# Kernel optimization log

Measured on AMD Instinct MI355X. Metric: run time of the kernel, lower is better.

## Reference

```python
import jax, jax.numpy as jnp
import numpy as np

N_NODES = 100_000
N_HYPEREDGES = 200_000
NNZ = 2_000_000
D = 64
H = 32
KEEP_RATIO = 0.5


def setup_inputs() -> dict:
    key = jax.random.key(0)
    ks = jax.random.split(key, 5)
    x = jax.random.normal(ks[0], (N_NODES, D), jnp.float32)
    V_idx = jax.random.randint(ks[1], (NNZ,), 0, N_NODES)
    E_idx = jax.random.randint(ks[2], (NNZ,), 0, N_HYPEREDGES)
    W1 = jax.random.normal(ks[3], (2 * D, H), jnp.float32) * (1.0 / np.sqrt(2 * D))
    b1 = jnp.zeros((H,), jnp.float32)
    W2 = jax.random.normal(ks[4], (H, 1), jnp.float32) * (1.0 / np.sqrt(H))
    b2 = jnp.zeros((1,), jnp.float32)
    return dict(x=x, V_idx=V_idx, E_idx=E_idx, W1=W1, b1=b1, W2=W2, b2=b2)


def _segment_mean(vals, idx, num_segments):
    # index_add sum / clamped count, matching reduce_incidence_to_edge / index_mean
    s = jax.ops.segment_sum(vals, idx, num_segments=num_segments)
    c = jax.ops.segment_sum(jnp.ones((vals.shape[0],), vals.dtype), idx,
                            num_segments=num_segments)
    c = jnp.clip(c, 1.0, None)
    if vals.ndim == 2:
        c = c[:, None]
    return s / c


def reference(x, V_idx, E_idx, W1, b1, W2, b2):
    xv = x[V_idx]                                   # [nnz, D] gather
    edge_feats = _segment_mean(xv, E_idx, N_HYPEREDGES)  # [E, D]
    pair = jnp.concatenate([xv, edge_feats[E_idx]], axis=-1)  # [nnz, 2D]
    h = jax.nn.relu(pair @ W1 + b1)                 # [nnz, H]
    probs = jax.nn.sigmoid((h @ W2 + b2)[:, 0])     # [nnz]

    k = max(1, int(KEEP_RATIO * NNZ))
    keep_ids = jax.lax.top_k(probs, k)[1]           # is_test=True path (deterministic)
    hard = jnp.zeros_like(probs).at[keep_ids].set(1.0)
    soft = jax.lax.stop_gradient(hard - probs) + probs  # straight-through

    edge_probs = _segment_mean(jax.lax.stop_gradient(probs), E_idx, N_HYPEREDGES)
    edge_soft = _segment_mean(soft, E_idx, N_HYPEREDGES)
    edge_hard = (_segment_mean(hard, E_idx, N_HYPEREDGES) > 0).astype(jnp.float32)
    return (probs, soft, hard, edge_probs, edge_soft, edge_hard)
```

## Files before the change

### kernel.cpp

```cpp
#include <hip/hip_runtime.h>
#include <math.h>

#define N_NODES   100000
#define N_EDGES   200000
#define NNZ       2000000
#define K_KEEP    1000000
#define BANDCAP   131072
#define TIECAP    4096
#define DELTA     1.0e-3f
#define SCAN_BLOCKS 196
#define USCALE (4294967296.0 / 4.0e-3)

#define OFF_PAB   ((size_t)0)
#define OFF_PB32  ((size_t)25600000)
#define OFF_VJ    ((size_t)33600000)
#define OFF_POS   ((size_t)49600000)
#define OFF_EOFF  ((size_t)57600000)
#define OFF_CUR   ((size_t)58400000)
#define OFF_BS    ((size_t)59200000)
#define OFF_BANDP ((size_t)59201024)
#define OFF_BANDJ ((size_t)59725312)
#define OFF_BANDE ((size_t)60249600)
#define OFF_BANDV ((size_t)60773888)
#define OFF_BANDK ((size_t)61298176)
#define OFF_TIEK  ((size_t)62346752)
#define OFF_TIEJ  ((size_t)62379520)
#define OFF_TIEP  ((size_t)62395904)
#define OFF_FLAG  ((size_t)62412288)
#define OFF_ECNT  ((size_t)64412288)
#define OFF_HIST  ((size_t)65212288)
#define OFF_ST    ((size_t)65245056)
#define ZERO_OFF  OFF_FLAG
#define ZERO_LEN  ((size_t)(65245312 - 62412288))

struct SelState {
    unsigned int B1;
    unsigned int rem1;
    float lo_edge, hi_edge;
    unsigned int bB1;
    unsigned int brem1;
    unsigned int bU0;
    unsigned int brem2;
    unsigned int _pad0[8];
    unsigned int n_hi;      unsigned int _pad1[15];
    unsigned int band_n;    unsigned int _pad2[15];
    unsigned int tie_n;     unsigned int _pad3[15];
};

__device__ __forceinline__ unsigned int band_u32(double key, float lo) {
    double t = (key - (double)lo) * USCALE;
    t = t < 0.0 ? 0.0 : (t > 4294967295.0 ? 4294967295.0 : t);
    return (unsigned int)t;
}

__global__ void proj_kernel(const float* __restrict__ x, const float* __restrict__ W1,
                            float2* __restrict__ p_ab2) {
    __shared__ float sW[128 * 32];
    __shared__ float sx[8][64];
    for (int t = threadIdx.x; t < 128 * 32; t += 256) sW[t] = W1[t];
    int base = blockIdx.x * 8;
    for (int t = threadIdx.x; t < 512; t += 256) {
        int n = t >> 6, d = t & 63;
        int g = base + n;
        sx[n][d] = (g < N_NODES) ? x[(size_t)g * 64 + d] : 0.f;
    }
    __syncthreads();
    int ln = threadIdx.x >> 5;
    int k  = threadIdx.x & 31;
    int node = base + ln;
    if (node >= N_NODES) return;
    float sa = 0.f, sb = 0.f;
    for (int d = 0; d < 64; ++d) {
        float xv = sx[ln][d];
        sa += xv * sW[d * 32 + k];
        sb += xv * sW[(64 + d) * 32 + k];
    }
    p_ab2[(size_t)node * 32 + k] = make_float2(sa, sb);
}

__global__ void count_kernel(const int* __restrict__ E, unsigned int* __restrict__ edge_cnt) {
    int j = blockIdx.x * 256 + threadIdx.x;
    if (j >= NNZ) return;
    atomicAdd(&edge_cnt[E[j]], 1u);
}

__global__ void scanA_kernel(const unsigned int* __restrict__ edge_cnt,
                             unsigned int* __restrict__ edge_off, unsigned int* __restrict__ bsums) {
    __shared__ unsigned int s[256];
    int tid = threadIdx.x;
    int base = blockIdx.x * 1024 + tid * 4;
    unsigned int v0 = (base + 0 < N_EDGES) ? edge_cnt[base + 0] : 0u;
    unsigned int v1 = (base + 1 < N_EDGES) ? edge_cnt[base + 1] : 0u;
    unsigned int v2 = (base + 2 < N_EDGES) ? edge_cnt[base + 2] : 0u;
    unsigned int v3 = (base + 3 < N_EDGES) ? edge_cnt[base + 3] : 0u;
    unsigned int tsum = v0 + v1 + v2 + v3;
    s[tid] = tsum;
    __syncthreads();
    for (int off = 1; off < 256; off <<= 1) {
        unsigned int t = (tid >= off) ? s[tid - off] : 0u;
        __syncthreads();
        s[tid] += t;
        __syncthreads();
    }
    unsigned int excl = s[tid] - tsum;
    if (base + 0 < N_EDGES) edge_off[base + 0] = excl;
    if (base + 1 < N_EDGES) edge_off[base + 1] = excl + v0;
    if (base + 2 < N_EDGES) edge_off[base + 2] = excl + v0 + v1;
    if (base + 3 < N_EDGES) edge_off[base + 3] = excl + v0 + v1 + v2;
    if (tid == 255) bsums[blockIdx.x] = s[255];
}

__global__ void scanB_kernel(unsigned int* __restrict__ bsums) {
    __shared__ unsigned int s[256];
    int tid = threadIdx.x;
    unsigned int v = (tid < SCAN_BLOCKS) ? bsums[tid] : 0u;
    s[tid] = v;
    __syncthreads();
    for (int off = 1; off < 256; off <<= 1) {
        unsigned int t = (tid >= off) ? s[tid - off] : 0u;
        __syncthreads();
        s[tid] += t;
        __syncthreads();
    }
    if (tid < SCAN_BLOCKS) bsums[tid] = s[tid] - v;
}

__global__ void scanC_kernel(unsigned int* __restrict__ edge_off, const unsigned int* __restrict__ bsums,
                             unsigned int* __restrict__ cursor) {
    int i = blockIdx.x * 256 + threadIdx.x;
    if (i >= N_EDGES) return;
    unsigned int o = edge_off[i] + bsums[i >> 10];
    edge_off[i] = o;
    cursor[i] = o;
}

__global__ void bucket_kernel(const int* __restrict__ V, const int* __restrict__ E,
                              unsigned int* __restrict__ cursor,
                              uint2* __restrict__ vj, unsigned int* __restrict__ pos) {
    unsigned int base = blockIdx.x * 2048 + threadIdx.x;
    int ev[8], vv[8];
    unsigned int pp[8];
    #pragma unroll
    for (int c = 0; c < 8; ++c) {
        unsigned int j = base + 256u * c;
        if (j < NNZ) { ev[c] = E[j]; vv[c] = V[j]; }
    }
    #pragma unroll
    for (int c = 0; c < 8; ++c) {
        unsigned int j = base + 256u * c;
        if (j < NNZ) pp[c] = atomicAdd(&cursor[ev[c]], 1u);
    }
    #pragma unroll
    for (int c = 0; c < 8; ++c) {
        unsigned int j = base + 256u * c;
        if (j < NNZ) {
            vj[pp[c]] = make_uint2((unsigned int)vv[c], j);
            pos[j] = pp[c];
        }
    }
}

__global__ void edge_logit_kernel(const uint2* __restrict__ vj,
                                  const unsigned int* __restrict__ edge_off,
                                  const unsigned int* __restrict__ edge_cnt,
                                  const float2* __restrict__ p_ab2,
                                  const float* __restrict__ b1, const float* __restrict__ W2,
                                  const float* __restrict__ b2,
                                  float* __restrict__ probs_b, float* __restrict__ o_ep) {
    __shared__ float sa[4][32 * 32];
    __shared__ float slog[4][32];
    __shared__ unsigned int sv[4][32];
    int e = blockIdx.x * 4 + (threadIdx.x >> 6);
    if (e >= N_EDGES) return;
    int w    = threadIdx.x >> 6;
    int lane = threadIdx.x & 63;
    int k    = lane & 31;
    unsigned int half = (unsigned int)(lane >> 5);

    unsigned int off = edge_off[e];
    unsigned int deg = edge_cnt[e];
    unsigned int mind = deg < 32u ? deg : 32u;

    if ((unsigned int)lane < mind) sv[w][lane] = vj[off + lane].x;

    float bacc = 0.f;
    unsigned int i = half;
    for (; i + 6u < mind; i += 8u) {
        unsigned int v0 = sv[w][i];
        unsigned int v1 = sv[w][i + 2u];
        unsigned int v2 = sv[w][i + 4u];
        unsigned int v3 = sv[w][i + 6u];
        float2 r0 = p_ab2[(size_t)v0 * 32u + k];
        float2 r1 = p_ab2[(size_t)v1 * 32u + k];
        float2 r2 = p_ab2[(size_t)v2 * 32u + k];
        float2 r3 = p_ab2[(size_t)v3 * 32u + k];
        sa[w][(i)      * 32 + k] = r0.x;
        sa[w][(i + 2u) * 32 + k] = r1.x;
        sa[w][(i + 4u) * 32 + k] = r2.x;
        sa[w][(i + 6u) * 32 + k] = r3.x;
        bacc += (r0.y + r1.y) + (r2.y + r3.y);
    }
    for (; i + 2u < mind; i += 4u) {
        unsigned int v0 = sv[w][i];
        unsigned int v1 = sv[w][i + 2u];
        float2 r0 = p_ab2[(size_t)v0 * 32u + k];
        float2 r1 = p_ab2[(size_t)v1 * 32u + k];
        sa[w][(i)      * 32 + k] = r0.x;
        sa[w][(i + 2u) * 32 + k] = r1.x;
        bacc += r0.y + r1.y;
    }
    for (; i < mind; i += 2u) {
        unsigned int v = sv[w][i];
        float2 r = p_ab2[(size_t)v * 32u + k];
        sa[w][i * 32 + k] = r.x;
        bacc += r.y;
    }
    for (i = 32u + half; i < deg; i += 2u) {
        unsigned int v = vj[off + i].x;
        bacc += p_ab2[(size_t)v * 32u + k].y;
    }

    float cc  = (float)(deg > 1u ? deg : 1u);
    float emk = (bacc + __shfl_xor(bacc, 32)) / cc + b1[k];
    float w2k = W2[k];
    float b2v = b2[0];
    float prsum = 0.f;

    i = half;
    for (; i + 2u < mind; i += 4u) {
        float h0 = sa[w][(i)      * 32 + k] + emk;
        float h1 = sa[w][(i + 2u) * 32 + k] + emk;
        h0 = h0 > 0.f ? h0 : 0.f;
        h1 = h1 > 0.f ? h1 : 0.f;
        float t0 = h0 * w2k;
        float t1 = h1 * w2k;
        #pragma unroll
        for (int o = 16; o > 0; o >>= 1) {
            t0 += __shfl_down(t0, o, 32);
            t1 += __shfl_down(t1, o, 32);
        }
        if (k == 0) { slog[w][i] = t0; slog[w][i + 2u] = t1; }
    }
    for (; i < mind; i += 2u) {
        float hk = sa[w][i * 32 + k] + emk;
        hk = hk > 0.f ? hk : 0.f;
        float t = hk * w2k;
        #pragma unroll
        for (int o = 16; o > 0; o >>= 1) t += __shfl_down(t, o, 32);
        if (k == 0) slog[w][i] = t;
    }
    if ((unsigned int)lane < mind) {
        float pr = 1.f / (1.f + __expf(-(slog[w][lane] + b2v)));
        probs_b[off + lane] = pr;
        prsum = pr;
    }
    for (i = 32u + half; i < deg; i += 2u) {
        unsigned int v = vj[off + i].x;
        float hk = p_ab2[(size_t)v * 32u + k].x + emk;
        hk = hk > 0.f ? hk : 0.f;
        float t = hk * w2k;
        #pragma unroll
        for (int o = 16; o > 0; o >>= 1) t += __shfl_down(t, o, 32);
        if (k == 0) {
            float pr = 1.f / (1.f + __expf(-(t + b2v)));
            probs_b[off + i] = pr;
            prsum += pr;
        }
    }
    #pragma unroll
    for (int o = 32; o > 0; o >>= 1) prsum += __shfl_down(prsum, o, 64);
    if (lane == 0) o_ep[e] = prsum / cc;
}

__global__ void hist1_kernel(const float* __restrict__ probs_b, unsigned int* __restrict__ hist) {
    __shared__ unsigned int lh[2048];
    for (int t = threadIdx.x; t < 2048; t += 256) lh[t] = 0;
    __syncthreads();
    for (unsigned int i = blockIdx.x * 256 + threadIdx.x; i < NNZ; i += gridDim.x * 256) {
        unsigned int key = __float_as_uint(probs_b[i]);
        atomicAdd(&lh[key >> 21], 1u);
    }
    __syncthreads();
    for (int t = threadIdx.x; t < 2048; t += 256)
        if (lh[t]) atomicAdd(&hist[t], lh[t]);
}

__global__ void hist2_kernel(const float* __restrict__ probs_b, const SelState* __restrict__ st,
                             unsigned int* __restrict__ hist) {
    __shared__ unsigned int lh[2048];
    for (int t = threadIdx.x; t < 2048; t += 256) lh[t] = 0;
    __syncthreads();
    unsigned int B1 = st->B1;
    for (unsigned int i = blockIdx.x * 256 + threadIdx.x; i < NNZ; i += gridDim.x * 256) {
        unsigned int key = __float_as_uint(probs_b[i]);
        if ((key >> 21) == B1) atomicAdd(&lh[(key >> 10) & 2047u], 1u);
    }
    __syncthreads();
    for (int t = threadIdx.x; t < 2048; t += 256)
        if (lh[t]) atomicAdd(&hist[2048 + t], lh[t]);
}

__global__ void scan_sel_kernel(const unsigned int* __restrict__ hist, SelState* __restrict__ st, int which) {
    __shared__ unsigned int csum[256];
    int t = threadIdx.x;
    unsigned int target = (which == 0) ? (unsigned int)K_KEEP : st->rem1;
    const unsigned int* h = hist + (which ? 2048 : 0);
    unsigned int b[8];
    unsigned int s = 0;
    #pragma unroll
    for (int i = 0; i < 8; ++i) { b[i] = h[t * 8 + i]; s += b[i]; }
    csum[t] = s;
    __syncthreads();
    for (int off = 1; off < 256; off <<= 1) {
        unsigned int v = (t + off < 256) ? csum[t + off] : 0u;
        __syncthreads();
        csum[t] += v;
        __syncthreads();
    }
    unsigned int above = csum[t] - s;
    if (above < target && target <= above + s) {
        unsigned int rem = target - above;
        unsigned int cum = 0;
        #pragma unroll
        for (int i = 7; i >= 0; --i) {
            if (rem <= cum + b[i]) {
                unsigned int bin = (unsigned int)(t * 8 + i);
                if (which == 0) { st->B1 = bin; st->rem1 = rem - cum; }
                else {
                    unsigned int P = (st->B1 << 21) | (bin << 10);
                    st->lo_edge = __uint_as_float(P) - DELTA;
                    st->hi_edge = __uint_as_float(P + 1024u) + DELTA;
                }
                break;
            }
            cum += b[i];
        }
    }
}

__global__ void bandsel_kernel(const float* __restrict__ probs_b, const int* __restrict__ E,
                               const uint2* __restrict__ vj,
                               SelState* __restrict__ st,
                               unsigned int* __restrict__ band_p, unsigned int* __restrict__ band_j,
                               unsigned int* __restrict__ band_e, unsigned int* __restrict__ band_v) {
    __shared__ unsigned int whi[4], wband[4];
    __shared__ unsigned int sbase, scur;
    float hi = st->hi_edge, lo = st->lo_edge;
    unsigned int nhi = 0, nband = 0;
    for (unsigned int p = blockIdx.x * 256 + threadIdx.x; p < NNZ; p += gridDim.x * 256) {
        float pk = probs_b[p];
        if (pk > hi) nhi++;
        else if (pk >= lo) nband++;
    }
    #pragma unroll
    for (int o = 32; o > 0; o >>= 1) {
        nhi   += __shfl_down(nhi, o);
        nband += __shfl_down(nband, o);
    }
    if ((threadIdx.x & 63) == 0) { whi[threadIdx.x >> 6] = nhi; wband[threadIdx.x >> 6] = nband; }
    __syncthreads();
    if (threadIdx.x == 0) {
        unsigned int th = whi[0] + whi[1] + whi[2] + whi[3];
        unsigned int tb = wband[0] + wband[1] + wband[2] + wband[3];
        if (th) atomicAdd(&st->n_hi, th);
        sbase = tb ? atomicAdd(&st->band_n, tb) : 0u;
        scur = 0;
    }
    __syncthreads();
    for (unsigned int p = blockIdx.x * 256 + threadIdx.x; p < NNZ; p += gridDim.x * 256) {
        float pk = probs_b[p];
        if (pk <= hi && pk >= lo) {
            unsigned int s = sbase + atomicAdd(&scur, 1u);
            if (s < BANDCAP) {
                uint2 t = vj[p];
                band_p[s] = p;
                band_j[s] = t.y;
                band_e[s] = (unsigned int)E[t.y];
                band_v[s] = t.x;
            }
        }
    }
}

__global__ void rescue_kernel(const uint2* __restrict__ vj,
                              const unsigned int* __restrict__ edge_off,
                              const unsigned int* __restrict__ edge_cnt,
                              const float* __restrict__ x, const float* __restrict__ W1,
                              const float* __restrict__ b1, const float* __restrict__ W2,
                              const float* __restrict__ b2,
                              const unsigned int* __restrict__ band_e,
                              const unsigned int* __restrict__ band_v,
                              const SelState* __restrict__ st,
                              unsigned long long* __restrict__ band_key) {
    unsigned int n = st->band_n; if (n > BANDCAP) n = BANDCAP;
    if (blockIdx.x * 8 >= n) return;
    __shared__ float sW[128 * 32];
    for (int t = threadIdx.x; t < 128 * 32; t += 256) sW[t] = W1[t];
    __syncthreads();
    unsigned int g = blockIdx.x * 8 + (threadIdx.x >> 5);
    if (g >= n) return;
    int k = threadIdx.x & 31;
    unsigned int v = band_v[g];
    unsigned int e = band_e[g];
    unsigned int off = edge_off[e];
    unsigned int deg = edge_cnt[e];

    const float* xv = x + (size_t)v * 64u;
    double a = 0.0;
    #pragma unroll 8
    for (int d = 0; d < 64; ++d) a += (double)xv[d] * (double)sW[d * 32 + k];
    double bsum = 0.0;
    for (unsigned int m = off; m < off + deg; ++m) {
        const float* xm = x + (size_t)vj[m].x * 64u;
        double acc = 0.0;
        #pragma unroll 8
        for (int d = 0; d < 64; ++d) acc += (double)xm[d] * (double)sW[(64 + d) * 32 + k];
        bsum += acc;
    }
    double cc = (double)(deg > 1u ? deg : 1u);
    double h = a + bsum / cc + (double)b1[k];
    h = h > 0.0 ? h : 0.0;
    double t = h * (double)W2[k];
    #pragma unroll
    for (int o = 16; o > 0; o >>= 1) t += __shfl_down(t, o, 32);
    if (k == 0) {
        double pr = 1.0 / (1.0 + exp(-(t + (double)b2[0])));
        band_key[g] = (unsigned long long)__double_as_longlong(pr);
    }
}

__global__ void bhist1_kernel(const unsigned long long* __restrict__ band_key,
                              const SelState* __restrict__ st, unsigned int* __restrict__ hist) {
    __shared__ unsigned int lh[2048];
    for (int t = threadIdx.x; t < 2048; t += 256) lh[t] = 0;
    __syncthreads();
    unsigned int n = st->band_n; if (n > BANDCAP) n = BANDCAP;
    float lo = st->lo_edge;
    for (unsigned int i = blockIdx.x * 256 + threadIdx.x; i < n; i += gridDim.x * 256) {
        unsigned int u = band_u32(__longlong_as_double((long long)band_key[i]), lo);
        atomicAdd(&lh[u >> 21], 1u);
    }
    __syncthreads();
    for (int t = threadIdx.x; t < 2048; t += 256)
        if (lh[t]) atomicAdd(&hist[4096 + t], lh[t]);
}

__global__ void bhist2_kernel(const unsigned long long* __restrict__ band_key,
                              const SelState* __restrict__ st, unsigned int* __restrict__ hist) {
    __shared__ unsigned int lh[2048];
    for (int t = threadIdx.x; t < 2048; t += 256) lh[t] = 0;
    __syncthreads();
    unsigned int n = st->band_n; if (n > BANDCAP) n = BANDCAP;
    float lo = st->lo_edge;
    unsigned int bB1 = st->bB1;
    for (unsigned int i = blockIdx.x * 256 + threadIdx.x; i < n; i += gridDim.x * 256) {
        unsigned int u = band_u32(__longlong_as_double((long long)band_key[i]), lo);
        if ((u >> 21) == bB1) atomicAdd(&lh[(u >> 10) & 2047u], 1u);
    }
    __syncthreads();
    for (int t = threadIdx.x; t < 2048; t += 256)
        if (lh[t]) atomicAdd(&hist[6144 + t], lh[t]);
}

__global__ void bscan_kernel(const unsigned int* __restrict__ hist, SelState* __restrict__ st, int which) {
    __shared__ unsigned int csum[256];
    int t = threadIdx.x;
    unsigned int target = (which == 0) ? ((unsigned int)K_KEEP - st->n_hi) : st->brem1;
    const unsigned int* h = hist + (which ? 6144 : 4096);
    unsigned int b[8];
    unsigned int s = 0;
    #pragma unroll
    for (int i = 0; i < 8; ++i) { b[i] = h[t * 8 + i]; s += b[i]; }
    csum[t] = s;
    __syncthreads();
    for (int off = 1; off < 256; off <<= 1) {
        unsigned int v = (t + off < 256) ? csum[t + off] : 0u;
        __syncthreads();
        csum[t] += v;
        __syncthreads();
    }
    unsigned int above = csum[t] - s;
    if (above < target && target <= above + s) {
        unsigned int rem = target - above;
        unsigned int cum = 0;
        #pragma unroll
        for (int i = 7; i >= 0; --i) {
            if (rem <= cum + b[i]) {
                unsigned int bin = (unsigned int)(t * 8 + i);
                if (which == 0) { st->bB1 = bin; st->brem1 = rem - cum; }
                else            { st->bU0 = (st->bB1 << 21) | (bin << 10); st->brem2 = rem - cum; }
                break;
            }
            cum += b[i];
        }
    }
}

__global__ void btie_kernel(const unsigned long long* __restrict__ band_key,
                            const unsigned int* __restrict__ band_j,
                            const unsigned int* __restrict__ band_p,
                            SelState* __restrict__ st, unsigned char* __restrict__ flag,
                            unsigned long long* __restrict__ tie_k,
                            unsigned int* __restrict__ tie_j, unsigned int* __restrict__ tie_p) {
    unsigned int n = st->band_n; if (n > BANDCAP) n = BANDCAP;
    unsigned int i = blockIdx.x * 256 + threadIdx.x;
    if (i >= n) return;
    float lo = st->lo_edge;
    unsigned int U0 = st->bU0;
    unsigned long long key = band_key[i];
    unsigned int u = band_u32(__longlong_as_double((long long)key), lo);
    if (u >= U0 + 1024u) {
        flag[band_p[i]] = 2u;
    } else if (u >= U0) {
        unsigned int s = atomicAdd(&st->tie_n, 1u);
        if (s < TIECAP) { tie_k[s] = key; tie_j[s] = band_j[i]; tie_p[s] = band_p[i]; }
    }
}

__global__ void btierank_kernel(const unsigned long long* __restrict__ tie_k,
                                const unsigned int* __restrict__ tie_j,
                                const unsigned int* __restrict__ tie_p,
                                const SelState* __restrict__ st, unsigned char* __restrict__ flag) {
    unsigned int n = st->tie_n; if (n > TIECAP) n = TIECAP;
    unsigned int need = st->brem2;
    for (unsigned int i = threadIdx.x; i < n; i += 256) {
        unsigned long long ki = tie_k[i];
        unsigned int ji = tie_j[i];
        unsigned int r = 0;
        for (unsigned int q = 0; q < n; ++q) {
            unsigned long long kq = tie_k[q];
            if (kq > ki || (kq == ki && tie_j[q] < ji)) r++;
        }
        if (r < need) flag[tie_p[i]] = 2u;
    }
}

__global__ void out_kernel(const float* __restrict__ probs_b, const unsigned char* __restrict__ flag,
                           const unsigned int* __restrict__ pos, const SelState* __restrict__ st,
                           float* __restrict__ o_probs, float* __restrict__ o_soft, float* __restrict__ o_hard) {
    unsigned int j = blockIdx.x * 256 + threadIdx.x;
    if (j >= NNZ) return;
    float hi = st->hi_edge;
    unsigned int p = pos[j];
    float pk = probs_b[p];
    float hb = (pk > hi || flag[p] == 2u) ? 1.f : 0.f;
    o_probs[j] = pk;
    o_soft[j]  = hb;
    o_hard[j]  = hb;
}

__global__ void edge_out_kernel(const float* __restrict__ probs_b, const unsigned char* __restrict__ flag,
                                const unsigned int* __restrict__ edge_off,
                                const unsigned int* __restrict__ edge_cnt,
                                const SelState* __restrict__ st,
                                float* __restrict__ o_es, float* __restrict__ o_eh) {
    unsigned int e = blockIdx.x * 256 + threadIdx.x;
    if (e >= N_EDGES) return;
    float hi = st->hi_edge;
    unsigned int off = edge_off[e], deg = edge_cnt[e];
    unsigned int cnt = 0;
    for (unsigned int i = 0; i < deg; ++i)
        cnt += (probs_b[off + i] > hi || flag[off + i] == 2u) ? 1u : 0u;
    float cc = (float)(deg > 1u ? deg : 1u);
    o_es[e] = (float)cnt / cc;
    o_eh[e] = cnt ? 1.f : 0.f;
}

extern "C" void kernel_launch(void* const* d_in, const int* in_sizes, int n_in,
                              void* d_out, int out_size, void* d_ws, size_t ws_size,
                              hipStream_t stream) {
    const float* x  = (const float*)d_in[0];
    const int*   V  = (const int*)d_in[1];
    const int*   E  = (const int*)d_in[2];
    const float* W1 = (const float*)d_in[3];
    const float* b1 = (const float*)d_in[4];
    const float* W2 = (const float*)d_in[5];
    const float* b2 = (const float*)d_in[6];

    float* out     = (float*)d_out;
    float* o_probs = out;
    float* o_soft  = out + NNZ;
    float* o_hard  = out + 2 * (size_t)NNZ;
    float* o_ep    = out + 3 * (size_t)NNZ;
    float* o_es    = out + 3 * (size_t)NNZ + N_EDGES;
    float* o_eh    = out + 3 * (size_t)NNZ + 2 * (size_t)N_EDGES;

    char* w = (char*)d_ws;
    float2*             p_ab2    = (float2*)(w + OFF_PAB);
    float*              probs_b  = (float*)(w + OFF_PB32);
    uint2*              vj       = (uint2*)(w + OFF_VJ);
    unsigned int*       pos      = (unsigned int*)(w + OFF_POS);
    unsigned int*       edge_off = (unsigned int*)(w + OFF_EOFF);
    unsigned int*       cursor   = (unsigned int*)(w + OFF_CUR);
    unsigned int*       bsums    = (unsigned int*)(w + OFF_BS);
    unsigned int*       band_p   = (unsigned int*)(w + OFF_BANDP);
    unsigned int*       band_j   = (unsigned int*)(w + OFF_BANDJ);
    unsigned int*       band_e   = (unsigned int*)(w + OFF_BANDE);
    unsigned int*       band_v   = (unsigned int*)(w + OFF_BANDV);
    unsigned long long* band_key = (unsigned long long*)(w + OFF_BANDK);
    unsigned long long* tie_k    = (unsigned long long*)(w + OFF_TIEK);
    unsigned int*       tie_j    = (unsigned int*)(w + OFF_TIEJ);
    unsigned int*       tie_p    = (unsigned int*)(w + OFF_TIEP);
    unsigned char*      flag     = (unsigned char*)(w + OFF_FLAG);
    unsigned int*       edge_cnt = (unsigned int*)(w + OFF_ECNT);
    unsigned int*       hist     = (unsigned int*)(w + OFF_HIST);
    SelState*           st       = (SelState*)(w + OFF_ST);

    hipMemsetAsync(w + ZERO_OFF, 0, ZERO_LEN, stream);

    proj_kernel<<<(N_NODES + 7) / 8, 256, 0, stream>>>(x, W1, p_ab2);

    count_kernel<<<(NNZ + 255) / 256, 256, 0, stream>>>(E, edge_cnt);
    scanA_kernel<<<SCAN_BLOCKS, 256, 0, stream>>>(edge_cnt, edge_off, bsums);
    scanB_kernel<<<1, 256, 0, stream>>>(bsums);
    scanC_kernel<<<(N_EDGES + 255) / 256, 256, 0, stream>>>(edge_off, bsums, cursor);
    bucket_kernel<<<(NNZ + 2047) / 2048, 256, 0, stream>>>(V, E, cursor, vj, pos);

    edge_logit_kernel<<<(N_EDGES + 3) / 4, 256, 0, stream>>>(vj, edge_off, edge_cnt,
                                                             p_ab2, b1, W2, b2, probs_b, o_ep);

    hist1_kernel<<<1024, 256, 0, stream>>>(probs_b, hist);
    scan_sel_kernel<<<1, 256, 0, stream>>>(hist, st, 0);
    hist2_kernel<<<1024, 256, 0, stream>>>(probs_b, st, hist);
    scan_sel_kernel<<<1, 256, 0, stream>>>(hist, st, 1);

    bandsel_kernel<<<1024, 256, 0, stream>>>(probs_b, E, vj, st,
                                             band_p, band_j, band_e, band_v);
    rescue_kernel<<<BANDCAP / 8, 256, 0, stream>>>(vj, edge_off, edge_cnt, x, W1, b1, W2, b2,
                                                   band_e, band_v, st, band_key);

    bhist1_kernel<<<64, 256, 0, stream>>>(band_key, st, hist);
    bscan_kernel<<<1, 256, 0, stream>>>(hist, st, 0);
    bhist2_kernel<<<64, 256, 0, stream>>>(band_key, st, hist);
    bscan_kernel<<<1, 256, 0, stream>>>(hist, st, 1);
    btie_kernel<<<BANDCAP / 256, 256, 0, stream>>>(band_key, band_j, band_p, st, flag,
                                                   tie_k, tie_j, tie_p);
    btierank_kernel<<<1, 256, 0, stream>>>(tie_k, tie_j, tie_p, st, flag);

    out_kernel<<<(NNZ + 255) / 256, 256, 0, stream>>>(probs_b, flag, pos, st, o_probs, o_soft, o_hard);
    edge_out_kernel<<<(N_EDGES + 255) / 256, 256, 0, stream>>>(probs_b, flag, edge_off, edge_cnt, st,
                                                               o_es, o_eh);
}
```

Baseline: 672.2 us.

## Compute bucket ranks during counting and scatter in edge-range passes

The counting kernel now records each incidence's rank within its edge from the atomicAdd return value, so the separate cursor atomics in the bucket kernel go away. A new scatter kernel writes vj positions as offset plus rank, split into 8 passes by edge range so each pass's scattered writes land in a smaller region for better cache locality. The pos array is dropped and out_kernel recomputes the position from E, rank and edge_off. This adds repeated streaming reads of E (eight passes) and extra gathers in out_kernel in exchange for fewer atomics and more localized writes.

```diff
diff --git a/kernel.cpp b/kernel.cpp
--- a/kernel.cpp
+++ b/kernel.cpp
@@ -11,10 +11,14 @@
 #define SCAN_BLOCKS 196
 #define USCALE (4294967296.0 / 4.0e-3)
 
+#define SC_PASSES 8
+#define SC_EPP    (N_EDGES / SC_PASSES)
+#define SC_BLOCKS 2048
+
 #define OFF_PAB   ((size_t)0)
 #define OFF_PB32  ((size_t)25600000)
 #define OFF_VJ    ((size_t)33600000)
-#define OFF_POS   ((size_t)49600000)
+#define OFF_RANK  ((size_t)49600000)
 #define OFF_EOFF  ((size_t)57600000)
 #define OFF_CUR   ((size_t)58400000)
 #define OFF_BS    ((size_t)59200000)
@@ -78,10 +82,26 @@
     p_ab2[(size_t)node * 32 + k] = make_float2(sa, sb);
 }
 
-__global__ void count_kernel(const int* __restrict__ E, unsigned int* __restrict__ edge_cnt) {
-    int j = blockIdx.x * 256 + threadIdx.x;
-    if (j >= NNZ) return;
-    atomicAdd(&edge_cnt[E[j]], 1u);
+__global__ void count_rank_kernel(const int* __restrict__ E, unsigned int* __restrict__ edge_cnt,
+                                  unsigned int* __restrict__ rank) {
+    unsigned int base = blockIdx.x * 2048 + threadIdx.x;
+    int ev[8];
+    unsigned int rr[8];
+    #pragma unroll
+    for (int c = 0; c < 8; ++c) {
+        unsigned int j = base + 256u * c;
+        if (j < NNZ) ev[c] = E[j];
+    }
+    #pragma unroll
+    for (int c = 0; c < 8; ++c) {
+        unsigned int j = base + 256u * c;
+        if (j < NNZ) rr[c] = atomicAdd(&edge_cnt[ev[c]], 1u);
+    }
+    #pragma unroll
+    for (int c = 0; c < 8; ++c) {
+        unsigned int j = base + 256u * c;
+        if (j < NNZ) rank[j] = rr[c];
+    }
 }
 
 __global__ void scanA_kernel(const unsigned int* __restrict__ edge_cnt,
@@ -125,37 +145,26 @@
     if (tid < SCAN_BLOCKS) bsums[tid] = s[tid] - v;
 }
 
-__global__ void scanC_kernel(unsigned int* __restrict__ edge_off, const unsigned int* __restrict__ bsums,
-                             unsigned int* __restrict__ cursor) {
+__global__ void scanC_kernel(unsigned int* __restrict__ edge_off, const unsigned int* __restrict__ bsums) {
     int i = blockIdx.x * 256 + threadIdx.x;
     if (i >= N_EDGES) return;
-    unsigned int o = edge_off[i] + bsums[i >> 10];
-    edge_off[i] = o;
-    cursor[i] = o;
-}
-
-__global__ void bucket_kernel(const int* __restrict__ V, const int* __restrict__ E,
-                              unsigned int* __restrict__ cursor,
-                              uint2* __restrict__ vj, unsigned int* __restrict__ pos) {
-    unsigned int base = blockIdx.x * 2048 + threadIdx.x;
-    int ev[8], vv[8];
-    unsigned int pp[8];
-    #pragma unroll
-    for (int c = 0; c < 8; ++c) {
-        unsigned int j = base + 256u * c;
-        if (j < NNZ) { ev[c] = E[j]; vv[c] = V[j]; }
-    }
-    #pragma unroll
-    for (int c = 0; c < 8; ++c) {
-        unsigned int j = base + 256u * c;
-        if (j < NNZ) pp[c] = atomicAdd(&cursor[ev[c]], 1u);
-    }
-    #pragma unroll
-    for (int c = 0; c < 8; ++c) {
-        unsigned int j = base + 256u * c;
-        if (j < NNZ) {
-            vj[pp[c]] = make_uint2((unsigned int)vv[c], j);
-            pos[j] = pp[c];
+    edge_off[i] = edge_off[i] + bsums[i >> 10];
+}
+
+__global__ void scatter_kernel(const int* __restrict__ V, const int* __restrict__ E,
+                               const unsigned int* __restrict__ edge_off,
+                               const unsigned int* __restrict__ rank,
+                               uint2* __restrict__ vj) {
+    unsigned int pass = blockIdx.x & 7u;
+    unsigned int q    = blockIdx.x >> 3;
+    unsigned int elo  = pass * SC_EPP;
+    const unsigned int stride = (SC_BLOCKS / 8) * 256;
+    for (unsigned int j = q * 256u + threadIdx.x; j < NNZ; j += stride) {
+        unsigned int e = (unsigned int)__builtin_nontemporal_load(E + j);
+        if (e - elo < (unsigned int)SC_EPP) {
+            unsigned int pp = edge_off[e] + __builtin_nontemporal_load(rank + j);
+            unsigned int v  = (unsigned int)__builtin_nontemporal_load(V + j);
+            vj[pp] = make_uint2(v, j);
         }
     }
 }
@@ -536,12 +545,13 @@
 }
 
 __global__ void out_kernel(const float* __restrict__ probs_b, const unsigned char* __restrict__ flag,
-                           const unsigned int* __restrict__ pos, const SelState* __restrict__ st,
+                           const int* __restrict__ E, const unsigned int* __restrict__ rank,
+                           const unsigned int* __restrict__ edge_off, const SelState* __restrict__ st,
                            float* __restrict__ o_probs, float* __restrict__ o_soft, float* __restrict__ o_hard) {
     unsigned int j = blockIdx.x * 256 + threadIdx.x;
     if (j >= NNZ) return;
     float hi = st->hi_edge;
-    unsigned int p = pos[j];
+    unsigned int p = edge_off[E[j]] + rank[j];
     float pk = probs_b[p];
     float hb = (pk > hi || flag[p] == 2u) ? 1.f : 0.f;
     o_probs[j] = pk;
@@ -589,9 +599,8 @@
     float2*             p_ab2    = (float2*)(w + OFF_PAB);
     float*              probs_b  = (float*)(w + OFF_PB32);
     uint2*              vj       = (uint2*)(w + OFF_VJ);
-    unsigned int*       pos      = (unsigned int*)(w + OFF_POS);
+    unsigned int*       rank     = (unsigned int*)(w + OFF_RANK);
     unsigned int*       edge_off = (unsigned int*)(w + OFF_EOFF);
-    unsigned int*       cursor   = (unsigned int*)(w + OFF_CUR);
     unsigned int*       bsums    = (unsigned int*)(w + OFF_BS);
     unsigned int*       band_p   = (unsigned int*)(w + OFF_BANDP);
     unsigned int*       band_j   = (unsigned int*)(w + OFF_BANDJ);
@@ -610,11 +619,11 @@
 
     proj_kernel<<<(N_NODES + 7) / 8, 256, 0, stream>>>(x, W1, p_ab2);
 
-    count_kernel<<<(NNZ + 255) / 256, 256, 0, stream>>>(E, edge_cnt);
+    count_rank_kernel<<<(NNZ + 2047) / 2048, 256, 0, stream>>>(E, edge_cnt, rank);
     scanA_kernel<<<SCAN_BLOCKS, 256, 0, stream>>>(edge_cnt, edge_off, bsums);
     scanB_kernel<<<1, 256, 0, stream>>>(bsums);
-    scanC_kernel<<<(N_EDGES + 255) / 256, 256, 0, stream>>>(edge_off, bsums, cursor);
-    bucket_kernel<<<(NNZ + 2047) / 2048, 256, 0, stream>>>(V, E, cursor, vj, pos);
+    scanC_kernel<<<(N_EDGES + 255) / 256, 256, 0, stream>>>(edge_off, bsums);
+    scatter_kernel<<<SC_BLOCKS, 256, 0, stream>>>(V, E, edge_off, rank, vj);
 
     edge_logit_kernel<<<(N_EDGES + 3) / 4, 256, 0, stream>>>(vj, edge_off, edge_cnt,
                                                              p_ab2, b1, W2, b2, probs_b, o_ep);
@@ -637,7 +646,8 @@
                                                    tie_k, tie_j, tie_p);
     btierank_kernel<<<1, 256, 0, stream>>>(tie_k, tie_j, tie_p, st, flag);
 
-    out_kernel<<<(NNZ + 255) / 256, 256, 0, stream>>>(probs_b, flag, pos, st, o_probs, o_soft, o_hard);
+    out_kernel<<<(NNZ + 255) / 256, 256, 0, stream>>>(probs_b, flag, E, rank, edge_off, st,
+                                                      o_probs, o_soft, o_hard);
     edge_out_kernel<<<(N_EDGES + 255) / 256, 256, 0, stream>>>(probs_b, flag, edge_off, edge_cnt, st,
                                                                o_es, o_eh);
 }
```

New measurement: 632.2 us. 6.0% less time.
